# Optimization experiments

Hardware: AMD Instinct MI355X
Metric: run time of the kernel (lower is better)

The kernel has to match this reference:

```python
import jax, jax.numpy as jnp
import numpy as np

T = 512        # sequence / max_length
I = 512        # input_dim
H = 1024       # hidden_size
O = 1          # output_size
L = 512        # max_length (attention logits)


def setup_inputs() -> dict:
    key = jax.random.key(0)
    ks = jax.random.split(key, 14)
    s = 0.02
    return {
        "input_seq": jax.random.normal(ks[0], (T, I), jnp.float32),
        "target_seq": jax.random.normal(ks[1], (T, O), jnp.float32),
        # encoder LSTM (input I -> hidden H), PyTorch gate order i,f,g,o
        "W_ih_e": jax.random.normal(ks[2], (4 * H, I), jnp.float32) * s,
        "W_hh_e": jax.random.normal(ks[3], (4 * H, H), jnp.float32) * s,
        "b_ih_e": jnp.zeros((4 * H,), jnp.float32),
        "b_hh_e": jnp.zeros((4 * H,), jnp.float32),
        # attention: Linear(2H -> L)
        "W_attn": jax.random.normal(ks[4], (L, 2 * H), jnp.float32) * s,
        "b_attn": jnp.zeros((L,), jnp.float32),
        # decoder LSTM (input 2H -> hidden H)
        "W_ih_d": jax.random.normal(ks[5], (4 * H, 2 * H), jnp.float32) * s,
        "W_hh_d": jax.random.normal(ks[6], (4 * H, H), jnp.float32) * s,
        "b_ih_d": jnp.zeros((4 * H,), jnp.float32),
        "b_hh_d": jnp.zeros((4 * H,), jnp.float32),
        # output Linear(H -> O)
        "W_out": jax.random.normal(ks[7], (O, H), jnp.float32) * s,
        "b_out": jnp.zeros((O,), jnp.float32),
    }


def _lstm_cell(x, h, c, Wih, Whh, bih, bhh):
    gates = Wih @ x + bih + Whh @ h + bhh          # [4H]
    i, f, g, o = jnp.split(gates, 4)
    c = jax.nn.sigmoid(f) * c + jax.nn.sigmoid(i) * jnp.tanh(g)
    h = jax.nn.sigmoid(o) * jnp.tanh(c)
    return h, c


def reference(input_seq, target_seq, W_ih_e, W_hh_e, b_ih_e, b_hh_e,
              W_attn, b_attn, W_ih_d, W_hh_d, b_ih_d, b_hh_d, W_out, b_out):
    Th = input_seq.shape[0]
    max_len = W_attn.shape[0]
    hid = W_hh_e.shape[1]

    def step(carry, xs):
        eh, ec, dh, dc, aw = carry
        x_t, i = xs
        eh, ec = _lstm_cell(x_t, eh, ec, W_ih_e, W_hh_e, b_ih_e, b_hh_e)
        energy = W_attn @ jnp.concatenate([eh, dh]) + b_attn   # [L]
        aw = aw.at[i].set(energy[i])
        aw = jax.nn.softmax(aw)                                 # re-softmaxed each step, as in source
        context = aw[i] * eh                                    # [H]
        din = jnp.concatenate([context, dh])                    # [2H]
        dh, dc = _lstm_cell(din, dh, dc, W_ih_d, W_hh_d, b_ih_d, b_hh_d)
        out_t = W_out @ dh + b_out                              # [O]
        return (eh, ec, dh, dc, aw), out_t

    z = jnp.zeros((hid,), input_seq.dtype)
    carry0 = (z, z, z, z, jnp.zeros((max_len,), input_seq.dtype))
    _, output_seq = jax.lax.scan(step, carry0, (input_seq, jnp.arange(Th)))
    return output_seq  # [T, O]
```

## Files before the change

### kernel.cpp

```cpp
#include <hip/hip_runtime.h>
#include <math.h>


#define T_STEPS 512
#define ENC_BLK 128
#define NBLK    256
#define SPIN_LIMIT 200000u
#define REP_STRIDE ((size_t)T_STEPS * 1024)

typedef float fv4 __attribute__((ext_vector_type(4)));

__device__ __forceinline__ float sigf(float x) { return 1.0f / (1.0f + expf(-x)); }

__device__ __forceinline__ unsigned ld_u(unsigned* p) {
  return __hip_atomic_load(p, __ATOMIC_RELAXED, __HIP_MEMORY_SCOPE_AGENT);
}
__device__ __forceinline__ void st_u(unsigned* p, unsigned v) {
  __hip_atomic_store(p, v, __ATOMIC_RELAXED, __HIP_MEMORY_SCOPE_AGENT);
}

__device__ __forceinline__ fv4 ld_bypass16(const float* p) {
  fv4 v;
  asm volatile("global_load_dwordx4 %0, %1, off sc0 sc1\n\t"
               "s_waitcnt vmcnt(0)"
               : "=&v"(v) : "v"(p) : "memory");
  return v;
}
__device__ __forceinline__ void st_bypass4(float* p, float v) {
  asm volatile("global_store_dword %0, %1, off sc0 sc1"
               :: "v"(p), "v"(v) : "memory");
}

__device__ __forceinline__ bool valid4(fv4 v) {
  return __float_as_uint(v.x) != 0xAAAAAAAAu && __float_as_uint(v.y) != 0xAAAAAAAAu &&
         __float_as_uint(v.z) != 0xAAAAAAAAu && __float_as_uint(v.w) != 0xAAAAAAAAu;
}

__device__ __forceinline__ fv4 poll_data(const float* p, unsigned* abortf, int* okp) {
  fv4 v;
  unsigned spins = 0;
  int ok = 1;
  for (;;) {
    v = ld_bypass16(p);
    if (valid4(v)) break;
    ++spins;
    if (spins > 4u) __builtin_amdgcn_s_sleep(1);
    if ((spins & 63u) == 0u) {
      if (ld_u(abortf) != 0u || spins > SPIN_LIMIT) { ok = 0; break; }
    }
  }
  *okp = ok;
  return v;
}

__global__ __launch_bounds__(256) void prep_gemm(const float* __restrict__ X,
                                                 const float* __restrict__ Wih,
                                                 const float* __restrict__ bih,
                                                 const float* __restrict__ bhh,
                                                 float* __restrict__ px,
                                                 unsigned* abortf) {
  if (blockIdx.x == 0 && blockIdx.y == 0 && threadIdx.x == 0) st_u(abortf, 0u);
  __shared__ float Ws[64][68];
  __shared__ float Xs[64][68];
  const int r0 = blockIdx.x * 64;
  const int t0 = blockIdx.y * 64;
  const int tid = threadIdx.x;
  const int tr = tid & 15;
  const int tc = tid >> 4;
  float acc[4][4] = {{0.f}};
  for (int k0 = 0; k0 < 512; k0 += 64) {
    __syncthreads();
    const int lr = tid >> 4;
    const int lc = (tid & 15) * 4;
#pragma unroll
    for (int rep = 0; rep < 4; rep++) {
      const int row = lr + rep * 16;
      const float4 wv = *(const float4*)&Wih[(size_t)(r0 + row) * 512 + k0 + lc];
      Ws[lc + 0][row] = wv.x; Ws[lc + 1][row] = wv.y;
      Ws[lc + 2][row] = wv.z; Ws[lc + 3][row] = wv.w;
      const float4 xv = *(const float4*)&X[(size_t)(t0 + row) * 512 + k0 + lc];
      Xs[row][lc + 0] = xv.x; Xs[row][lc + 1] = xv.y;
      Xs[row][lc + 2] = xv.z; Xs[row][lc + 3] = xv.w;
    }
    __syncthreads();
    for (int kk = 0; kk < 64; kk++) {
      float a[4], x[4];
#pragma unroll
      for (int i = 0; i < 4; i++) a[i] = Ws[kk][tr * 4 + i];
#pragma unroll
      for (int j = 0; j < 4; j++) x[j] = Xs[tc * 4 + j][kk];
#pragma unroll
      for (int i = 0; i < 4; i++)
#pragma unroll
        for (int j = 0; j < 4; j++) acc[i][j] += a[i] * x[j];
    }
  }
#pragma unroll
  for (int i = 0; i < 4; i++) {
    const int r = r0 + tr * 4 + i;
    const int g = r >> 10, h = r & 1023;
    const float bsum = bih[r] + bhh[r];
#pragma unroll
    for (int j = 0; j < 4; j++) {
      const int t = t0 + tc * 4 + j;
      px[((size_t)t * 1024 + h) * 4 + g] = acc[i][j] + bsum;
    }
  }
}

__global__ __launch_bounds__(256, 1) void lstm_persist(
    const float* __restrict__ Whhe, const float* __restrict__ Wattn,
    const float* __restrict__ battn, const float* __restrict__ Wihd,
    const float* __restrict__ Whhd, const float* __restrict__ bihd,
    const float* __restrict__ bhhd, const float* __restrict__ Wout,
    const float* __restrict__ bout, const float* __restrict__ px,
    float* ehbuf, float* dhbuf, int nrep, unsigned* abortf, float* out) {
  __shared__ float4 xbuf[256];
  __shared__ float4 dbuf[256];
  __shared__ float  aw[512];
  __shared__ float  GA[32];
  __shared__ float  GB[32];
  __shared__ float  redE[4];
  __shared__ float  redE2[4];
  __shared__ float  red[8];
  __shared__ float  red2[4];
  __shared__ float  bd[32];
  __shared__ int    sbad;

  const int b    = blockIdx.x;
  const int tid  = threadIdx.x;
  const int w    = tid >> 6;
  const int lane = tid & 63;
  const int jj   = lane & 7;
  const int seg  = lane >> 3;
  const size_t myrep = (size_t)(b & (nrep - 1)) * REP_STRIDE;

  if (b < ENC_BLK) {
    const int e = b;
    const int r = (w << 10) + (e << 3) + jj;
    float4 we[32];
#pragma unroll
    for (int k = 0; k < 32; k++) {
      const int m = (k + seg) & 31;
      we[k] = *(const float4*)&Whhe[(size_t)r * 1024 + seg * 128 + m * 4];
    }
    xbuf[tid] = make_float4(0.f, 0.f, 0.f, 0.f);
    if (tid == 0) sbad = 0;
    float ec = 0.f;
    __syncthreads();

    for (int t = 0; t < T_STEPS; t++) {
      float pxv = 0.f;
      if (seg == 0) pxv = px[((size_t)t * 1024 + (e << 3) + jj) * 4 + w];
      float ge = 0.f;
#pragma unroll
      for (int k = 0; k < 32; k++) {
        const int m = (k + seg) & 31;
        const float4 x = xbuf[seg * 32 + m];
        ge += we[k].x * x.x + we[k].y * x.y + we[k].z * x.z + we[k].w * x.w;
      }
      ge += __shfl_xor(ge, 8, 64);
      ge += __shfl_xor(ge, 16, 64);
      ge += __shfl_xor(ge, 32, 64);
      if (seg == 0) GA[(w << 3) + jj] = ge + pxv;
      __syncthreads();
      if (tid < 8) {
        const float gi = GA[tid], gf = GA[8 + tid], gg = GA[16 + tid], go = GA[24 + tid];
        const float c = sigf(gf) * ec + sigf(gi) * tanhf(gg);
        ec = c;
        const float h = sigf(go) * tanhf(c);
        for (int rp = 0; rp < nrep; rp++)
          st_bypass4(&ehbuf[(size_t)rp * REP_STRIDE + (size_t)t * 1024 + (e << 3) + tid], h);
      }
      int ok;
      const fv4 ev = poll_data(&ehbuf[myrep + (size_t)t * 1024 + tid * 4], abortf, &ok);
      if (!ok) { st_u(abortf, 1u); sbad = 1; }
      xbuf[tid] = make_float4(ev.x, ev.y, ev.z, ev.w);
      __syncthreads();
      if (sbad) break;
    }
  } else {
    const int d = b - ENC_BLK;
    const int r = (w << 10) + (d << 3) + jj;
    float4 w1[32], wr[32];
#pragma unroll
    for (int k = 0; k < 32; k++) {
      const int m = (k + seg) & 31;
      w1[k] = *(const float4*)&Wihd[(size_t)r * 2048 + seg * 128 + m * 4];
      const float4 a = *(const float4*)&Wihd[(size_t)r * 2048 + 1024 + seg * 128 + m * 4];
      const float4 c = *(const float4*)&Whhd[(size_t)r * 1024 + seg * 128 + m * 4];
      wr[k] = make_float4(a.x + c.x, a.y + c.y, a.z + c.z, a.w + c.w);
    }
    if (tid < 32) {
      const int g = tid >> 3, j = tid & 7;
      bd[tid] = bihd[(g << 10) + (d << 3) + j] + bhhd[(g << 10) + (d << 3) + j];
    }
    xbuf[tid] = make_float4(0.f, 0.f, 0.f, 0.f);
    dbuf[tid] = make_float4(0.f, 0.f, 0.f, 0.f);
    aw[tid] = 0.f; aw[tid + 256] = 0.f;
    if (tid == 0) sbad = 0;
    float dc = 0.f;
    const float4 wo = *(const float4*)&Wout[tid * 4];
    const float boutv = bout[0];
    __syncthreads();

    bool failed = false;
    for (int t = 0; t < T_STEPS; t++) {
      const float4 wae = *(const float4*)&Wattn[(size_t)t * 2048 + tid * 4];
      const float4 wad = *(const float4*)&Wattn[(size_t)t * 2048 + 1024 + tid * 4];
      const float battn_t = battn[t];
      const float ex0 = expf(aw[tid]);
      const float ex1 = expf(aw[tid + 256]);
      float so = ((tid == t) ? 0.f : ex0) + ((tid + 256 == t) ? 0.f : ex1);
#pragma unroll
      for (int mk = 1; mk <= 32; mk <<= 1) so += __shfl_xor(so, mk, 64);
      if (lane == 0) red[w] = so;

      int ok1;
      const fv4 ev = poll_data(&ehbuf[myrep + (size_t)t * 1024 + tid * 4], abortf, &ok1);
      if (!ok1) { st_u(abortf, 1u); sbad = 1; }
      float epe = wae.x * ev.x + wae.y * ev.y + wae.z * ev.z + wae.w * ev.w;
#pragma unroll
      for (int mk = 1; mk <= 32; mk <<= 1) epe += __shfl_xor(epe, mk, 64);
      if (lane == 0) redE[w] = epe;
      xbuf[tid] = make_float4(ev.x, ev.y, ev.z, ev.w);
      __syncthreads();
      if (sbad) { failed = true; break; }

      float g1 = 0.f;
#pragma unroll
      for (int k = 0; k < 32; k++) {
        const int m = (k + seg) & 31;
        const float4 x = xbuf[seg * 32 + m];
        g1 += w1[k].x * x.x + w1[k].y * x.y + w1[k].z * x.z + w1[k].w * x.w;
      }
      g1 += __shfl_xor(g1, 8, 64); g1 += __shfl_xor(g1, 16, 64); g1 += __shfl_xor(g1, 32, 64);
      if (seg == 0) GA[(w << 3) + jj] = g1;

      fv4 dv = {0.f, 0.f, 0.f, 0.f};
      float epd = 0.f;
      if (t > 0) {
        int ok2;
        dv = poll_data(&dhbuf[myrep + (size_t)(t - 1) * 1024 + tid * 4], abortf, &ok2);
        if (!ok2) { st_u(abortf, 1u); sbad = 1; }
        epd = wad.x * dv.x + wad.y * dv.y + wad.z * dv.z + wad.w * dv.w;
      }
#pragma unroll
      for (int mk = 1; mk <= 32; mk <<= 1) epd += __shfl_xor(epd, mk, 64);
      if (lane == 0) redE2[w] = epd;
      dbuf[tid] = make_float4(dv.x, dv.y, dv.z, dv.w);
      __syncthreads();
      if (sbad) { failed = true; break; }

      float g2 = 0.f;
#pragma unroll
      for (int k = 0; k < 32; k++) {
        const int m = (k + seg) & 31;
        const float4 dd = dbuf[seg * 32 + m];
        g2 += wr[k].x * dd.x + wr[k].y * dd.y + wr[k].z * dd.z + wr[k].w * dd.w;
      }
      g2 += __shfl_xor(g2, 8, 64); g2 += __shfl_xor(g2, 16, 64); g2 += __shfl_xor(g2, 32, 64);
      if (seg == 0) GB[(w << 3) + jj] = g2;

      const float sum_other = red[0] + red[1] + red[2] + red[3];
      const float e_t = redE[0] + redE[1] + redE[2] + redE[3] +
                        redE2[0] + redE2[1] + redE2[2] + redE2[3] + battn_t;
      const float exden = expf(e_t);
      const float inv = 1.f / (sum_other + exden);
      aw[tid] = ((tid == t) ? exden : ex0) * inv;
      aw[tid + 256] = ((tid + 256 == t) ? exden : ex1) * inv;
      const float awt = exden * inv;
      __syncthreads();

      if (tid < 8) {
        const float gi = awt * GA[tid]      + GB[tid]      + bd[tid];
        const float gf = awt * GA[8 + tid]  + GB[8 + tid]  + bd[8 + tid];
        const float gg = awt * GA[16 + tid] + GB[16 + tid] + bd[16 + tid];
        const float go = awt * GA[24 + tid] + GB[24 + tid] + bd[24 + tid];
        const float c = sigf(gf) * dc + sigf(gi) * tanhf(gg);
        dc = c;
        const float h = sigf(go) * tanhf(c);
        for (int rp = 0; rp < nrep; rp++)
          st_bypass4(&dhbuf[(size_t)rp * REP_STRIDE + (size_t)t * 1024 + (d << 3) + tid], h);
      }
    }

    if (!failed) {
#pragma unroll
      for (int i = 0; i < 4; i++) {
        const int t = d * 4 + i;
        int ok;
        const fv4 dv = poll_data(&dhbuf[myrep + (size_t)t * 1024 + tid * 4], abortf, &ok);
        if (!ok) break;
        float op = wo.x * dv.x + wo.y * dv.y + wo.z * dv.z + wo.w * dv.w;
#pragma unroll
        for (int mk = 1; mk <= 32; mk <<= 1) op += __shfl_xor(op, mk, 64);
        if (lane == 0) red2[w] = op;
        __syncthreads();
        if (tid == 0) out[t] = red2[0] + red2[1] + red2[2] + red2[3] + boutv;
        __syncthreads();
      }
    }
  }
}

extern "C" void kernel_launch(void* const* d_in, const int* in_sizes, int n_in,
                              void* d_out, int out_size, void* d_ws, size_t ws_size,
                              hipStream_t stream) {
  const float* X     = (const float*)d_in[0];
  const float* Wihe  = (const float*)d_in[2];
  const float* Whhe  = (const float*)d_in[3];
  const float* bihe  = (const float*)d_in[4];
  const float* bhhe  = (const float*)d_in[5];
  const float* Wattn = (const float*)d_in[6];
  const float* battn = (const float*)d_in[7];
  const float* Wihd  = (const float*)d_in[8];
  const float* Whhd  = (const float*)d_in[9];
  const float* bihd  = (const float*)d_in[10];
  const float* bhhd  = (const float*)d_in[11];
  const float* Wo    = (const float*)d_in[12];
  const float* bo    = (const float*)d_in[13];
  float* out = (float*)d_out;

  const size_t px_elems = (size_t)T_STEPS * 1024 * 4;
  int nrep = 8;
  size_t need;
  for (;; nrep >>= 1) {
    need = (px_elems + 2 * (size_t)nrep * REP_STRIDE) * sizeof(float) + sizeof(unsigned);
    if (need <= ws_size || nrep == 1) break;
  }
  if (ws_size < need) return;

  float* ws    = (float*)d_ws;
  float* px    = ws;
  float* ehbuf = px + px_elems;
  float* dhbuf = ehbuf + (size_t)nrep * REP_STRIDE;
  unsigned* abortf = (unsigned*)(dhbuf + (size_t)nrep * REP_STRIDE);

  prep_gemm<<<dim3(64, 8), 256, 0, stream>>>(X, Wihe, bihe, bhhe, px, abortf);
  lstm_persist<<<NBLK, 256, 0, stream>>>(
      Whhe, Wattn, battn, Wihd, Whhd, bihd, bhhd, Wo, bo, px, ehbuf, dhbuf,
      nrep, abortf, out);
}
```

Measured before the change: 2.114 ms.

## Replace LDS gate exchange with shuffles, pipeline polling, drop replicas and abort flag

Row mapping changes so all four gates of a hidden unit sit in one wavefront. Gate combination therefore uses cross-lane shuffles instead of shared-memory arrays plus a block barrier, which removes a __syncthreads per step in both encoder and decoder. Polling moves to an inline-asm loop that keeps two sets of bypass loads in flight, and drops the sleep and the global abort-flag checks. The replicated eh/dh buffers are collapsed to a single copy, which cuts store traffic but concentrates all reads on one location. Double-buffered shared arrays keep the one remaining barrier per step safe.

```diff
diff --git a/kernel.cpp b/kernel.cpp
--- a/kernel.cpp
+++ b/kernel.cpp
@@ -5,61 +5,90 @@
 #define T_STEPS 512
 #define ENC_BLK 128
 #define NBLK    256
-#define SPIN_LIMIT 200000u
-#define REP_STRIDE ((size_t)T_STEPS * 1024)
 
 typedef float fv4 __attribute__((ext_vector_type(4)));
 
 __device__ __forceinline__ float sigf(float x) { return 1.0f / (1.0f + expf(-x)); }
 
-__device__ __forceinline__ unsigned ld_u(unsigned* p) {
-  return __hip_atomic_load(p, __ATOMIC_RELAXED, __HIP_MEMORY_SCOPE_AGENT);
-}
-__device__ __forceinline__ void st_u(unsigned* p, unsigned v) {
-  __hip_atomic_store(p, v, __ATOMIC_RELAXED, __HIP_MEMORY_SCOPE_AGENT);
-}
-
-__device__ __forceinline__ fv4 ld_bypass16(const float* p) {
-  fv4 v;
-  asm volatile("global_load_dwordx4 %0, %1, off sc0 sc1\n\t"
-               "s_waitcnt vmcnt(0)"
-               : "=&v"(v) : "v"(p) : "memory");
-  return v;
-}
 __device__ __forceinline__ void st_bypass4(float* p, float v) {
   asm volatile("global_store_dword %0, %1, off sc0 sc1"
                :: "v"(p), "v"(v) : "memory");
 }
 
-__device__ __forceinline__ bool valid4(fv4 v) {
-  return __float_as_uint(v.x) != 0xAAAAAAAAu && __float_as_uint(v.y) != 0xAAAAAAAAu &&
-         __float_as_uint(v.z) != 0xAAAAAAAAu && __float_as_uint(v.w) != 0xAAAAAAAAu;
-}
-
-__device__ __forceinline__ fv4 poll_data(const float* p, unsigned* abortf, int* okp) {
-  fv4 v;
-  unsigned spins = 0;
-  int ok = 1;
-  for (;;) {
-    v = ld_bypass16(p);
-    if (valid4(v)) break;
-    ++spins;
-    if (spins > 4u) __builtin_amdgcn_s_sleep(1);
-    if ((spins & 63u) == 0u) {
-      if (ld_u(abortf) != 0u || spins > SPIN_LIMIT) { ok = 0; break; }
-    }
-  }
-  *okp = ok;
-  return v;
+__device__ __forceinline__ fv4 poll_pipe(const float* p, int* okp) {
+  float a0, a1, a2, a3, b0, b1, b2, b3;
+  unsigned flag, cnt;
+  asm volatile(
+      "s_mov_b32 %8, 0\n\t"
+      "s_mov_b32 %9, 0\n\t"
+      "global_load_dword %0, %10, off sc0 sc1\n\t"
+      "global_load_dword %1, %10, off offset:4 sc0 sc1\n\t"
+      "global_load_dword %2, %10, off offset:8 sc0 sc1\n\t"
+      "global_load_dword %3, %10, off offset:12 sc0 sc1\n\t"
+      "PLA%=:\n\t"
+      "global_load_dword %4, %10, off sc0 sc1\n\t"
+      "global_load_dword %5, %10, off offset:4 sc0 sc1\n\t"
+      "global_load_dword %6, %10, off offset:8 sc0 sc1\n\t"
+      "global_load_dword %7, %10, off offset:12 sc0 sc1\n\t"
+      "s_waitcnt vmcnt(4)\n\t"
+      "v_cmp_eq_u32 vcc, 0xaaaaaaaa, %0\n\t"
+      "s_cbranch_vccnz PRB%=\n\t"
+      "v_cmp_eq_u32 vcc, 0xaaaaaaaa, %1\n\t"
+      "s_cbranch_vccnz PRB%=\n\t"
+      "v_cmp_eq_u32 vcc, 0xaaaaaaaa, %2\n\t"
+      "s_cbranch_vccnz PRB%=\n\t"
+      "v_cmp_eq_u32 vcc, 0xaaaaaaaa, %3\n\t"
+      "s_cbranch_vccnz PRB%=\n\t"
+      "s_waitcnt vmcnt(0)\n\t"
+      "s_branch PDONE%=\n\t"
+      "PRB%=:\n\t"
+      "s_add_u32 %9, %9, 1\n\t"
+      "s_cmp_lt_u32 %9, 0xc350\n\t"
+      "s_cbranch_scc0 PTO%=\n\t"
+      "global_load_dword %0, %10, off sc0 sc1\n\t"
+      "global_load_dword %1, %10, off offset:4 sc0 sc1\n\t"
+      "global_load_dword %2, %10, off offset:8 sc0 sc1\n\t"
+      "global_load_dword %3, %10, off offset:12 sc0 sc1\n\t"
+      "s_waitcnt vmcnt(4)\n\t"
+      "v_cmp_eq_u32 vcc, 0xaaaaaaaa, %4\n\t"
+      "s_cbranch_vccnz PRA%=\n\t"
+      "v_cmp_eq_u32 vcc, 0xaaaaaaaa, %5\n\t"
+      "s_cbranch_vccnz PRA%=\n\t"
+      "v_cmp_eq_u32 vcc, 0xaaaaaaaa, %6\n\t"
+      "s_cbranch_vccnz PRA%=\n\t"
+      "v_cmp_eq_u32 vcc, 0xaaaaaaaa, %7\n\t"
+      "s_cbranch_vccnz PRA%=\n\t"
+      "s_waitcnt vmcnt(0)\n\t"
+      "v_mov_b32 %0, %4\n\t"
+      "v_mov_b32 %1, %5\n\t"
+      "v_mov_b32 %2, %6\n\t"
+      "v_mov_b32 %3, %7\n\t"
+      "s_branch PDONE%=\n\t"
+      "PRA%=:\n\t"
+      "s_add_u32 %9, %9, 1\n\t"
+      "s_cmp_lt_u32 %9, 0xc350\n\t"
+      "s_cbranch_scc0 PTO%=\n\t"
+      "s_branch PLA%=\n\t"
+      "PTO%=:\n\t"
+      "s_mov_b32 %8, 1\n\t"
+      "s_waitcnt vmcnt(0)\n\t"
+      "PDONE%=:"
+      : "=&v"(a0), "=&v"(a1), "=&v"(a2), "=&v"(a3),
+        "=&v"(b0), "=&v"(b1), "=&v"(b2), "=&v"(b3),
+        "=&s"(flag), "=&s"(cnt)
+      : "v"(p)
+      : "vcc", "scc", "memory");
+  *okp = (flag == 0);
+  fv4 r;
+  r.x = a0; r.y = a1; r.z = a2; r.w = a3;
+  return r;
 }
 
 __global__ __launch_bounds__(256) void prep_gemm(const float* __restrict__ X,
                                                  const float* __restrict__ Wih,
                                                  const float* __restrict__ bih,
                                                  const float* __restrict__ bhh,
-                                                 float* __restrict__ px,
-                                                 unsigned* abortf) {
-  if (blockIdx.x == 0 && blockIdx.y == 0 && threadIdx.x == 0) st_u(abortf, 0u);
+                                                 float* __restrict__ px) {
   __shared__ float Ws[64][68];
   __shared__ float Xs[64][68];
   const int r0 = blockIdx.x * 64;
@@ -114,74 +143,72 @@
     const float* __restrict__ Whhd, const float* __restrict__ bihd,
     const float* __restrict__ bhhd, const float* __restrict__ Wout,
     const float* __restrict__ bout, const float* __restrict__ px,
-    float* ehbuf, float* dhbuf, int nrep, unsigned* abortf, float* out) {
-  __shared__ float4 xbuf[256];
-  __shared__ float4 dbuf[256];
+    float* ehbuf, float* dhbuf, float* out) {
+  __shared__ float4 xbufE[2][256];
+  __shared__ float4 xbufD[256];
+  __shared__ float4 dbufD[256];
   __shared__ float  aw[512];
-  __shared__ float  GA[32];
-  __shared__ float  GB[32];
-  __shared__ float  redE[4];
-  __shared__ float  redE2[4];
-  __shared__ float  red[8];
+  __shared__ float  redE[2][4];
+  __shared__ float  redE2[2][4];
+  __shared__ float  red[2][4];
   __shared__ float  red2[4];
-  __shared__ float  bd[32];
   __shared__ int    sbad;
 
-  const int b    = blockIdx.x;
-  const int tid  = threadIdx.x;
-  const int w    = tid >> 6;
-  const int lane = tid & 63;
-  const int jj   = lane & 7;
-  const int seg  = lane >> 3;
-  const size_t myrep = (size_t)(b & (nrep - 1)) * REP_STRIDE;
+  const int b     = blockIdx.x;
+  const int tid   = threadIdx.x;
+  const int w     = tid >> 6;
+  const int lane  = tid & 63;
+  const int idx   = lane & 7;
+  const int g     = idx >> 1;
+  const int jc    = lane & 1;
+  const int seg   = lane >> 3;
 
   if (b < ENC_BLK) {
     const int e = b;
-    const int r = (w << 10) + (e << 3) + jj;
+    const int r = (g << 10) + (e << 3) + 2 * w + (idx & 1);
     float4 we[32];
 #pragma unroll
     for (int k = 0; k < 32; k++) {
       const int m = (k + seg) & 31;
       we[k] = *(const float4*)&Whhe[(size_t)r * 1024 + seg * 128 + m * 4];
     }
-    xbuf[tid] = make_float4(0.f, 0.f, 0.f, 0.f);
+    xbufE[0][tid] = make_float4(0.f, 0.f, 0.f, 0.f);
     if (tid == 0) sbad = 0;
     float ec = 0.f;
     __syncthreads();
 
     for (int t = 0; t < T_STEPS; t++) {
-      float pxv = 0.f;
-      if (seg == 0) pxv = px[((size_t)t * 1024 + (e << 3) + jj) * 4 + w];
+      const int par = t & 1;
       float ge = 0.f;
 #pragma unroll
       for (int k = 0; k < 32; k++) {
         const int m = (k + seg) & 31;
-        const float4 x = xbuf[seg * 32 + m];
+        const float4 x = xbufE[par][seg * 32 + m];
         ge += we[k].x * x.x + we[k].y * x.y + we[k].z * x.z + we[k].w * x.w;
       }
+      if (lane < 8)
+        ge += px[((size_t)t * 1024 + (e << 3) + 2 * w + (idx & 1)) * 4 + g];
       ge += __shfl_xor(ge, 8, 64);
       ge += __shfl_xor(ge, 16, 64);
       ge += __shfl_xor(ge, 32, 64);
-      if (seg == 0) GA[(w << 3) + jj] = ge + pxv;
-      __syncthreads();
-      if (tid < 8) {
-        const float gi = GA[tid], gf = GA[8 + tid], gg = GA[16 + tid], go = GA[24 + tid];
+      const float gi = __shfl(ge, jc, 64), gf = __shfl(ge, 2 + jc, 64);
+      const float gg = __shfl(ge, 4 + jc, 64), go = __shfl(ge, 6 + jc, 64);
+      if (lane < 2) {
         const float c = sigf(gf) * ec + sigf(gi) * tanhf(gg);
         ec = c;
         const float h = sigf(go) * tanhf(c);
-        for (int rp = 0; rp < nrep; rp++)
-          st_bypass4(&ehbuf[(size_t)rp * REP_STRIDE + (size_t)t * 1024 + (e << 3) + tid], h);
+        st_bypass4(&ehbuf[(size_t)t * 1024 + (e << 3) + 2 * w + lane], h);
       }
       int ok;
-      const fv4 ev = poll_data(&ehbuf[myrep + (size_t)t * 1024 + tid * 4], abortf, &ok);
-      if (!ok) { st_u(abortf, 1u); sbad = 1; }
-      xbuf[tid] = make_float4(ev.x, ev.y, ev.z, ev.w);
+      const fv4 ev = poll_pipe(&ehbuf[(size_t)t * 1024 + tid * 4], &ok);
+      if (!ok) sbad = 1;
+      xbufE[par ^ 1][tid] = make_float4(ev.x, ev.y, ev.z, ev.w);
       __syncthreads();
       if (sbad) break;
     }
   } else {
     const int d = b - ENC_BLK;
-    const int r = (w << 10) + (d << 3) + jj;
+    const int r = (g << 10) + (d << 3) + 2 * w + (idx & 1);
     float4 w1[32], wr[32];
 #pragma unroll
     for (int k = 0; k < 32; k++) {
@@ -191,12 +218,7 @@
       const float4 c = *(const float4*)&Whhd[(size_t)r * 1024 + seg * 128 + m * 4];
       wr[k] = make_float4(a.x + c.x, a.y + c.y, a.z + c.z, a.w + c.w);
     }
-    if (tid < 32) {
-      const int g = tid >> 3, j = tid & 7;
-      bd[tid] = bihd[(g << 10) + (d << 3) + j] + bhhd[(g << 10) + (d << 3) + j];
-    }
-    xbuf[tid] = make_float4(0.f, 0.f, 0.f, 0.f);
-    dbuf[tid] = make_float4(0.f, 0.f, 0.f, 0.f);
+    const float bdreg = bihd[r] + bhhd[r];
     aw[tid] = 0.f; aw[tid + 256] = 0.f;
     if (tid == 0) sbad = 0;
     float dc = 0.f;
@@ -206,6 +228,7 @@
 
     bool failed = false;
     for (int t = 0; t < T_STEPS; t++) {
+      const int par = t & 1;
       const float4 wae = *(const float4*)&Wattn[(size_t)t * 2048 + tid * 4];
       const float4 wad = *(const float4*)&Wattn[(size_t)t * 2048 + 1024 + tid * 4];
       const float battn_t = battn[t];
@@ -214,16 +237,16 @@
       float so = ((tid == t) ? 0.f : ex0) + ((tid + 256 == t) ? 0.f : ex1);
 #pragma unroll
       for (int mk = 1; mk <= 32; mk <<= 1) so += __shfl_xor(so, mk, 64);
-      if (lane == 0) red[w] = so;
+      if (lane == 0) red[par][w] = so;
 
       int ok1;
-      const fv4 ev = poll_data(&ehbuf[myrep + (size_t)t * 1024 + tid * 4], abortf, &ok1);
-      if (!ok1) { st_u(abortf, 1u); sbad = 1; }
+      const fv4 ev = poll_pipe(&ehbuf[(size_t)t * 1024 + tid * 4], &ok1);
+      if (!ok1) sbad = 1;
       float epe = wae.x * ev.x + wae.y * ev.y + wae.z * ev.z + wae.w * ev.w;
 #pragma unroll
       for (int mk = 1; mk <= 32; mk <<= 1) epe += __shfl_xor(epe, mk, 64);
-      if (lane == 0) redE[w] = epe;
-      xbuf[tid] = make_float4(ev.x, ev.y, ev.z, ev.w);
+      if (lane == 0) redE[par][w] = epe;
+      xbufD[tid] = make_float4(ev.x, ev.y, ev.z, ev.w);
       __syncthreads();
       if (sbad) { failed = true; break; }
 
@@ -231,24 +254,25 @@
 #pragma unroll
       for (int k = 0; k < 32; k++) {
         const int m = (k + seg) & 31;
-        const float4 x = xbuf[seg * 32 + m];
+        const float4 x = xbufD[seg * 32 + m];
         g1 += w1[k].x * x.x + w1[k].y * x.y + w1[k].z * x.z + w1[k].w * x.w;
       }
-      g1 += __shfl_xor(g1, 8, 64); g1 += __shfl_xor(g1, 16, 64); g1 += __shfl_xor(g1, 32, 64);
-      if (seg == 0) GA[(w << 3) + jj] = g1;
+      g1 += __shfl_xor(g1, 8, 64);
+      g1 += __shfl_xor(g1, 16, 64);
+      g1 += __shfl_xor(g1, 32, 64);
 
       fv4 dv = {0.f, 0.f, 0.f, 0.f};
       float epd = 0.f;
       if (t > 0) {
         int ok2;
-        dv = poll_data(&dhbuf[myrep + (size_t)(t - 1) * 1024 + tid * 4], abortf, &ok2);
-        if (!ok2) { st_u(abortf, 1u); sbad = 1; }
+        dv = poll_pipe(&dhbuf[(size_t)(t - 1) * 1024 + tid * 4], &ok2);
+        if (!ok2) sbad = 1;
         epd = wad.x * dv.x + wad.y * dv.y + wad.z * dv.z + wad.w * dv.w;
       }
 #pragma unroll
       for (int mk = 1; mk <= 32; mk <<= 1) epd += __shfl_xor(epd, mk, 64);
-      if (lane == 0) redE2[w] = epd;
-      dbuf[tid] = make_float4(dv.x, dv.y, dv.z, dv.w);
+      if (lane == 0) redE2[par][w] = epd;
+      dbufD[tid] = make_float4(dv.x, dv.y, dv.z, dv.w);
       __syncthreads();
       if (sbad) { failed = true; break; }
 
@@ -256,33 +280,31 @@
 #pragma unroll
       for (int k = 0; k < 32; k++) {
         const int m = (k + seg) & 31;
-        const float4 dd = dbuf[seg * 32 + m];
+        const float4 dd = dbufD[seg * 32 + m];
         g2 += wr[k].x * dd.x + wr[k].y * dd.y + wr[k].z * dd.z + wr[k].w * dd.w;
       }
-      g2 += __shfl_xor(g2, 8, 64); g2 += __shfl_xor(g2, 16, 64); g2 += __shfl_xor(g2, 32, 64);
-      if (seg == 0) GB[(w << 3) + jj] = g2;
-
-      const float sum_other = red[0] + red[1] + red[2] + red[3];
-      const float e_t = redE[0] + redE[1] + redE[2] + redE[3] +
-                        redE2[0] + redE2[1] + redE2[2] + redE2[3] + battn_t;
+      g2 += __shfl_xor(g2, 8, 64);
+      g2 += __shfl_xor(g2, 16, 64);
+      g2 += __shfl_xor(g2, 32, 64);
+
+      const float e_t = redE[par][0] + redE[par][1] + redE[par][2] + redE[par][3] +
+                        redE2[par][0] + redE2[par][1] + redE2[par][2] + redE2[par][3] +
+                        battn_t;
       const float exden = expf(e_t);
-      const float inv = 1.f / (sum_other + exden);
-      aw[tid] = ((tid == t) ? exden : ex0) * inv;
-      aw[tid + 256] = ((tid + 256 == t) ? exden : ex1) * inv;
+      const float inv = 1.f / (red[par][0] + red[par][1] + red[par][2] + red[par][3] + exden);
       const float awt = exden * inv;
-      __syncthreads();
-
-      if (tid < 8) {
-        const float gi = awt * GA[tid]      + GB[tid]      + bd[tid];
-        const float gf = awt * GA[8 + tid]  + GB[8 + tid]  + bd[8 + tid];
-        const float gg = awt * GA[16 + tid] + GB[16 + tid] + bd[16 + tid];
-        const float go = awt * GA[24 + tid] + GB[24 + tid] + bd[24 + tid];
+
+      const float v = awt * g1 + g2 + bdreg;
+      const float gi = __shfl(v, jc, 64), gf = __shfl(v, 2 + jc, 64);
+      const float gg = __shfl(v, 4 + jc, 64), go = __shfl(v, 6 + jc, 64);
+      if (lane < 2) {
         const float c = sigf(gf) * dc + sigf(gi) * tanhf(gg);
         dc = c;
         const float h = sigf(go) * tanhf(c);
-        for (int rp = 0; rp < nrep; rp++)
-          st_bypass4(&dhbuf[(size_t)rp * REP_STRIDE + (size_t)t * 1024 + (d << 3) + tid], h);
-      }
+        st_bypass4(&dhbuf[(size_t)t * 1024 + (d << 3) + 2 * w + lane], h);
+      }
+      aw[tid] = ((tid == t) ? exden : ex0) * inv;
+      aw[tid + 256] = ((tid + 256 == t) ? exden : ex1) * inv;
     }
 
     if (!failed) {
@@ -290,7 +312,7 @@
       for (int i = 0; i < 4; i++) {
         const int t = d * 4 + i;
         int ok;
-        const fv4 dv = poll_data(&dhbuf[myrep + (size_t)t * 1024 + tid * 4], abortf, &ok);
+        const fv4 dv = poll_pipe(&dhbuf[(size_t)t * 1024 + tid * 4], &ok);
         if (!ok) break;
         float op = wo.x * dv.x + wo.y * dv.y + wo.z * dv.z + wo.w * dv.w;
 #pragma unroll
@@ -322,23 +344,14 @@
   const float* bo    = (const float*)d_in[13];
   float* out = (float*)d_out;
 
-  const size_t px_elems = (size_t)T_STEPS * 1024 * 4;
-  int nrep = 8;
-  size_t need;
-  for (;; nrep >>= 1) {
-    need = (px_elems + 2 * (size_t)nrep * REP_STRIDE) * sizeof(float) + sizeof(unsigned);
-    if (need <= ws_size || nrep == 1) break;
-  }
-  if (ws_size < need) return;
-
   float* ws    = (float*)d_ws;
   float* px    = ws;
-  float* ehbuf = px + px_elems;
-  float* dhbuf = ehbuf + (size_t)nrep * REP_STRIDE;
-  unsigned* abortf = (unsigned*)(dhbuf + (size_t)nrep * REP_STRIDE);
-
-  prep_gemm<<<dim3(64, 8), 256, 0, stream>>>(X, Wihe, bihe, bhhe, px, abortf);
+  float* ehbuf = px + (size_t)T_STEPS * 1024 * 4;
+  float* dhbuf = ehbuf + (size_t)T_STEPS * 1024;
+  const size_t need = ((size_t)T_STEPS * 1024 * 6) * sizeof(float);
+  if (ws_size < need) return;
+
+  prep_gemm<<<dim3(64, 8), 256, 0, stream>>>(X, Wihe, bihe, bhhe, px);
   lstm_persist<<<NBLK, 256, 0, stream>>>(
-      Whhe, Wattn, battn, Wihd, Whhd, bihd, bhhd, Wo, bo, px, ehbuf, dhbuf,
-      nrep, abortf, out);
-}
+      Whhe, Wattn, battn, Wihd, Whhd, bihd, bhhd, Wo, bo, px, ehbuf, dhbuf, out);
+}
```

Result: slower. 2.887 ms (+36.6%).

## Double persistent block width to 512 threads and drop replicated hidden-state buffers

Applied to the files above, without the earlier changes.

Raises the persistent LSTM kernel from 256 to 512 threads per block, halving each thread's register-resident weight slice (16 instead of 32 float4 per matrix) and splitting the dot product over 16 lanes instead of 8. Removes the nrep replication of the encoder/decoder hidden-state buffers and the abort-flag machinery, so each producer writes one copy and all consumers poll a single location. The new poll routine keeps two outstanding cache-bypassing loads in flight and drops the sleep, aiming to cut per-step handoff latency. In exchange it adds more polling contention on one buffer, and the timeout no longer propagates across blocks through a shared flag.

```diff
diff --git a/kernel.cpp b/kernel.cpp
--- a/kernel.cpp
+++ b/kernel.cpp
@@ -5,27 +5,13 @@
 #define T_STEPS 512
 #define ENC_BLK 128
 #define NBLK    256
-#define SPIN_LIMIT 200000u
-#define REP_STRIDE ((size_t)T_STEPS * 1024)
+#define NTHR    512
+#define POLL_LIMIT 30000u
 
 typedef float fv4 __attribute__((ext_vector_type(4)));
 
 __device__ __forceinline__ float sigf(float x) { return 1.0f / (1.0f + expf(-x)); }
 
-__device__ __forceinline__ unsigned ld_u(unsigned* p) {
-  return __hip_atomic_load(p, __ATOMIC_RELAXED, __HIP_MEMORY_SCOPE_AGENT);
-}
-__device__ __forceinline__ void st_u(unsigned* p, unsigned v) {
-  __hip_atomic_store(p, v, __ATOMIC_RELAXED, __HIP_MEMORY_SCOPE_AGENT);
-}
-
-__device__ __forceinline__ fv4 ld_bypass16(const float* p) {
-  fv4 v;
-  asm volatile("global_load_dwordx4 %0, %1, off sc0 sc1\n\t"
-               "s_waitcnt vmcnt(0)"
-               : "=&v"(v) : "v"(p) : "memory");
-  return v;
-}
 __device__ __forceinline__ void st_bypass4(float* p, float v) {
   asm volatile("global_store_dword %0, %1, off sc0 sc1"
                :: "v"(p), "v"(v) : "memory");
@@ -36,30 +22,28 @@
          __float_as_uint(v.z) != 0xAAAAAAAAu && __float_as_uint(v.w) != 0xAAAAAAAAu;
 }
 
-__device__ __forceinline__ fv4 poll_data(const float* p, unsigned* abortf, int* okp) {
-  fv4 v;
-  unsigned spins = 0;
+__device__ __forceinline__ fv4 poll2(const float* p, int* okp) {
+  fv4 a, b;
   int ok = 1;
-  for (;;) {
-    v = ld_bypass16(p);
-    if (valid4(v)) break;
-    ++spins;
-    if (spins > 4u) __builtin_amdgcn_s_sleep(1);
-    if ((spins & 63u) == 0u) {
-      if (ld_u(abortf) != 0u || spins > SPIN_LIMIT) { ok = 0; break; }
-    }
+  asm volatile("global_load_dwordx4 %0, %1, off sc0 sc1" : "=v"(a) : "v"(p) : "memory");
+  for (unsigned it = 0;; ++it) {
+    asm volatile("global_load_dwordx4 %0, %1, off sc0 sc1" : "=v"(b) : "v"(p) : "memory");
+    asm volatile("s_waitcnt vmcnt(1)" : "+v"(a) :: "memory");
+    if (valid4(a)) { asm volatile("s_waitcnt vmcnt(0)" ::: "memory"); break; }
+    asm volatile("global_load_dwordx4 %0, %1, off sc0 sc1" : "=v"(a) : "v"(p) : "memory");
+    asm volatile("s_waitcnt vmcnt(1)" : "+v"(b) :: "memory");
+    if (valid4(b)) { asm volatile("s_waitcnt vmcnt(0)" ::: "memory"); a = b; break; }
+    if (it > POLL_LIMIT) { ok = 0; asm volatile("s_waitcnt vmcnt(0)" ::: "memory"); break; }
   }
   *okp = ok;
-  return v;
+  return a;
 }
 
 __global__ __launch_bounds__(256) void prep_gemm(const float* __restrict__ X,
                                                  const float* __restrict__ Wih,
                                                  const float* __restrict__ bih,
                                                  const float* __restrict__ bhh,
-                                                 float* __restrict__ px,
-                                                 unsigned* abortf) {
-  if (blockIdx.x == 0 && blockIdx.y == 0 && threadIdx.x == 0) st_u(abortf, 0u);
+                                                 float* __restrict__ px) {
   __shared__ float Ws[64][68];
   __shared__ float Xs[64][68];
   const int r0 = blockIdx.x * 64;
@@ -108,168 +92,181 @@
   }
 }
 
-__global__ __launch_bounds__(256, 1) void lstm_persist(
+__global__ __launch_bounds__(512, 1) void lstm_persist(
     const float* __restrict__ Whhe, const float* __restrict__ Wattn,
     const float* __restrict__ battn, const float* __restrict__ Wihd,
     const float* __restrict__ Whhd, const float* __restrict__ bihd,
     const float* __restrict__ bhhd, const float* __restrict__ Wout,
     const float* __restrict__ bout, const float* __restrict__ px,
-    float* ehbuf, float* dhbuf, int nrep, unsigned* abortf, float* out) {
+    float* ehbuf, float* dhbuf, float* out) {
   __shared__ float4 xbuf[256];
   __shared__ float4 dbuf[256];
   __shared__ float  aw[512];
   __shared__ float  GA[32];
   __shared__ float  GB[32];
+  __shared__ float  bd[32];
   __shared__ float  redE[4];
   __shared__ float  redE2[4];
   __shared__ float  red[8];
   __shared__ float  red2[4];
-  __shared__ float  bd[32];
   __shared__ int    sbad;
 
   const int b    = blockIdx.x;
   const int tid  = threadIdx.x;
   const int w    = tid >> 6;
   const int lane = tid & 63;
-  const int jj   = lane & 7;
-  const int seg  = lane >> 3;
-  const size_t myrep = (size_t)(b & (nrep - 1)) * REP_STRIDE;
+  const int ri   = lane & 3;
+  const int s16  = lane >> 2;
+  const int g    = w >> 1;
+  const int j    = ((w & 1) << 2) + ri;
 
   if (b < ENC_BLK) {
     const int e = b;
-    const int r = (w << 10) + (e << 3) + jj;
-    float4 we[32];
-#pragma unroll
-    for (int k = 0; k < 32; k++) {
-      const int m = (k + seg) & 31;
-      we[k] = *(const float4*)&Whhe[(size_t)r * 1024 + seg * 128 + m * 4];
-    }
-    xbuf[tid] = make_float4(0.f, 0.f, 0.f, 0.f);
+    const int r = (g << 10) + (e << 3) + j;
+    float4 we[16];
+#pragma unroll
+    for (int k = 0; k < 16; k++) {
+      const int m = (k + s16) & 15;
+      we[k] = *(const float4*)&Whhe[(size_t)r * 1024 + s16 * 64 + m * 4];
+    }
+    if (tid < 256) xbuf[tid] = make_float4(0.f, 0.f, 0.f, 0.f);
     if (tid == 0) sbad = 0;
     float ec = 0.f;
     __syncthreads();
 
     for (int t = 0; t < T_STEPS; t++) {
-      float pxv = 0.f;
-      if (seg == 0) pxv = px[((size_t)t * 1024 + (e << 3) + jj) * 4 + w];
       float ge = 0.f;
 #pragma unroll
-      for (int k = 0; k < 32; k++) {
-        const int m = (k + seg) & 31;
-        const float4 x = xbuf[seg * 32 + m];
+      for (int k = 0; k < 16; k++) {
+        const int m = (k + s16) & 15;
+        const float4 x = xbuf[s16 * 16 + m];
         ge += we[k].x * x.x + we[k].y * x.y + we[k].z * x.z + we[k].w * x.w;
       }
+      if (s16 == 0) ge += px[((size_t)t * 1024 + (e << 3) + j) * 4 + g];
+      ge += __shfl_xor(ge, 4, 64);
       ge += __shfl_xor(ge, 8, 64);
       ge += __shfl_xor(ge, 16, 64);
       ge += __shfl_xor(ge, 32, 64);
-      if (seg == 0) GA[(w << 3) + jj] = ge + pxv;
+      if (lane < 4) GA[w * 4 + lane] = ge;
       __syncthreads();
       if (tid < 8) {
         const float gi = GA[tid], gf = GA[8 + tid], gg = GA[16 + tid], go = GA[24 + tid];
         const float c = sigf(gf) * ec + sigf(gi) * tanhf(gg);
         ec = c;
         const float h = sigf(go) * tanhf(c);
-        for (int rp = 0; rp < nrep; rp++)
-          st_bypass4(&ehbuf[(size_t)rp * REP_STRIDE + (size_t)t * 1024 + (e << 3) + tid], h);
-      }
-      int ok;
-      const fv4 ev = poll_data(&ehbuf[myrep + (size_t)t * 1024 + tid * 4], abortf, &ok);
-      if (!ok) { st_u(abortf, 1u); sbad = 1; }
-      xbuf[tid] = make_float4(ev.x, ev.y, ev.z, ev.w);
+        st_bypass4(&ehbuf[(size_t)t * 1024 + (e << 3) + tid], h);
+      }
+      int ok = 1;
+      if (tid < 256) {
+        const fv4 ev = poll2(&ehbuf[(size_t)t * 1024 + tid * 4], &ok);
+        xbuf[tid] = make_float4(ev.x, ev.y, ev.z, ev.w);
+      }
+      if (!ok) sbad = 1;
       __syncthreads();
       if (sbad) break;
     }
   } else {
     const int d = b - ENC_BLK;
-    const int r = (w << 10) + (d << 3) + jj;
-    float4 w1[32], wr[32];
-#pragma unroll
-    for (int k = 0; k < 32; k++) {
-      const int m = (k + seg) & 31;
-      w1[k] = *(const float4*)&Wihd[(size_t)r * 2048 + seg * 128 + m * 4];
-      const float4 a = *(const float4*)&Wihd[(size_t)r * 2048 + 1024 + seg * 128 + m * 4];
-      const float4 c = *(const float4*)&Whhd[(size_t)r * 1024 + seg * 128 + m * 4];
+    const int r = (g << 10) + (d << 3) + j;
+    float4 w1[16], wr[16];
+#pragma unroll
+    for (int k = 0; k < 16; k++) {
+      const int m = (k + s16) & 15;
+      w1[k] = *(const float4*)&Wihd[(size_t)r * 2048 + s16 * 64 + m * 4];
+      const float4 a = *(const float4*)&Wihd[(size_t)r * 2048 + 1024 + s16 * 64 + m * 4];
+      const float4 c = *(const float4*)&Whhd[(size_t)r * 1024 + s16 * 64 + m * 4];
       wr[k] = make_float4(a.x + c.x, a.y + c.y, a.z + c.z, a.w + c.w);
     }
     if (tid < 32) {
-      const int g = tid >> 3, j = tid & 7;
-      bd[tid] = bihd[(g << 10) + (d << 3) + j] + bhhd[(g << 10) + (d << 3) + j];
-    }
-    xbuf[tid] = make_float4(0.f, 0.f, 0.f, 0.f);
-    dbuf[tid] = make_float4(0.f, 0.f, 0.f, 0.f);
-    aw[tid] = 0.f; aw[tid + 256] = 0.f;
+      const int gg2 = tid >> 3, jj2 = tid & 7;
+      bd[tid] = bihd[(gg2 << 10) + (d << 3) + jj2] + bhhd[(gg2 << 10) + (d << 3) + jj2];
+    }
+    aw[tid] = 0.f;
+    if (tid < 256) {
+      xbuf[tid] = make_float4(0.f, 0.f, 0.f, 0.f);
+      dbuf[tid] = make_float4(0.f, 0.f, 0.f, 0.f);
+    }
     if (tid == 0) sbad = 0;
     float dc = 0.f;
-    const float4 wo = *(const float4*)&Wout[tid * 4];
+    float4 wo = make_float4(0.f, 0.f, 0.f, 0.f);
+    if (tid < 256) wo = *(const float4*)&Wout[tid * 4];
     const float boutv = bout[0];
     __syncthreads();
 
     bool failed = false;
     for (int t = 0; t < T_STEPS; t++) {
-      const float4 wae = *(const float4*)&Wattn[(size_t)t * 2048 + tid * 4];
-      const float4 wad = *(const float4*)&Wattn[(size_t)t * 2048 + 1024 + tid * 4];
       const float battn_t = battn[t];
       const float ex0 = expf(aw[tid]);
-      const float ex1 = expf(aw[tid + 256]);
-      float so = ((tid == t) ? 0.f : ex0) + ((tid + 256 == t) ? 0.f : ex1);
+      float so = (tid == t) ? 0.f : ex0;
 #pragma unroll
       for (int mk = 1; mk <= 32; mk <<= 1) so += __shfl_xor(so, mk, 64);
       if (lane == 0) red[w] = so;
 
-      int ok1;
-      const fv4 ev = poll_data(&ehbuf[myrep + (size_t)t * 1024 + tid * 4], abortf, &ok1);
-      if (!ok1) { st_u(abortf, 1u); sbad = 1; }
-      float epe = wae.x * ev.x + wae.y * ev.y + wae.z * ev.z + wae.w * ev.w;
+      float4 wae = make_float4(0.f, 0.f, 0.f, 0.f);
+      float4 wad = make_float4(0.f, 0.f, 0.f, 0.f);
+      float epe = 0.f;
+      int ok1 = 1;
+      if (tid < 256) {
+        wae = *(const float4*)&Wattn[(size_t)t * 2048 + tid * 4];
+        wad = *(const float4*)&Wattn[(size_t)t * 2048 + 1024 + tid * 4];
+        const fv4 ev = poll2(&ehbuf[(size_t)t * 1024 + tid * 4], &ok1);
+        epe = wae.x * ev.x + wae.y * ev.y + wae.z * ev.z + wae.w * ev.w;
+        xbuf[tid] = make_float4(ev.x, ev.y, ev.z, ev.w);
+      }
+      if (!ok1) sbad = 1;
 #pragma unroll
       for (int mk = 1; mk <= 32; mk <<= 1) epe += __shfl_xor(epe, mk, 64);
-      if (lane == 0) redE[w] = epe;
-      xbuf[tid] = make_float4(ev.x, ev.y, ev.z, ev.w);
+      if (lane == 0 && w < 4) redE[w] = epe;
       __syncthreads();
       if (sbad) { failed = true; break; }
 
       float g1 = 0.f;
 #pragma unroll
-      for (int k = 0; k < 32; k++) {
-        const int m = (k + seg) & 31;
-        const float4 x = xbuf[seg * 32 + m];
+      for (int k = 0; k < 16; k++) {
+        const int m = (k + s16) & 15;
+        const float4 x = xbuf[s16 * 16 + m];
         g1 += w1[k].x * x.x + w1[k].y * x.y + w1[k].z * x.z + w1[k].w * x.w;
       }
-      g1 += __shfl_xor(g1, 8, 64); g1 += __shfl_xor(g1, 16, 64); g1 += __shfl_xor(g1, 32, 64);
-      if (seg == 0) GA[(w << 3) + jj] = g1;
-
-      fv4 dv = {0.f, 0.f, 0.f, 0.f};
+      g1 += __shfl_xor(g1, 4, 64);
+      g1 += __shfl_xor(g1, 8, 64);
+      g1 += __shfl_xor(g1, 16, 64);
+      g1 += __shfl_xor(g1, 32, 64);
+      if (lane < 4) GA[w * 4 + lane] = g1;
+
       float epd = 0.f;
-      if (t > 0) {
-        int ok2;
-        dv = poll_data(&dhbuf[myrep + (size_t)(t - 1) * 1024 + tid * 4], abortf, &ok2);
-        if (!ok2) { st_u(abortf, 1u); sbad = 1; }
+      int ok2 = 1;
+      if (t > 0 && tid < 256) {
+        const fv4 dv = poll2(&dhbuf[(size_t)(t - 1) * 1024 + tid * 4], &ok2);
         epd = wad.x * dv.x + wad.y * dv.y + wad.z * dv.z + wad.w * dv.w;
-      }
+        dbuf[tid] = make_float4(dv.x, dv.y, dv.z, dv.w);
+      }
+      if (!ok2) sbad = 1;
 #pragma unroll
       for (int mk = 1; mk <= 32; mk <<= 1) epd += __shfl_xor(epd, mk, 64);
-      if (lane == 0) redE2[w] = epd;
-      dbuf[tid] = make_float4(dv.x, dv.y, dv.z, dv.w);
+      if (lane == 0 && w < 4) redE2[w] = epd;
       __syncthreads();
       if (sbad) { failed = true; break; }
 
       float g2 = 0.f;
 #pragma unroll
-      for (int k = 0; k < 32; k++) {
-        const int m = (k + seg) & 31;
-        const float4 dd = dbuf[seg * 32 + m];
+      for (int k = 0; k < 16; k++) {
+        const int m = (k + s16) & 15;
+        const float4 dd = dbuf[s16 * 16 + m];
         g2 += wr[k].x * dd.x + wr[k].y * dd.y + wr[k].z * dd.z + wr[k].w * dd.w;
       }
-      g2 += __shfl_xor(g2, 8, 64); g2 += __shfl_xor(g2, 16, 64); g2 += __shfl_xor(g2, 32, 64);
-      if (seg == 0) GB[(w << 3) + jj] = g2;
-
-      const float sum_other = red[0] + red[1] + red[2] + red[3];
+      g2 += __shfl_xor(g2, 4, 64);
+      g2 += __shfl_xor(g2, 8, 64);
+      g2 += __shfl_xor(g2, 16, 64);
+      g2 += __shfl_xor(g2, 32, 64);
+      if (lane < 4) GB[w * 4 + lane] = g2;
+
       const float e_t = redE[0] + redE[1] + redE[2] + redE[3] +
                         redE2[0] + redE2[1] + redE2[2] + redE2[3] + battn_t;
       const float exden = expf(e_t);
-      const float inv = 1.f / (sum_other + exden);
+      const float inv = 1.f / (red[0] + red[1] + red[2] + red[3] +
+                               red[4] + red[5] + red[6] + red[7] + exden);
+      const float awt = exden * inv;
       aw[tid] = ((tid == t) ? exden : ex0) * inv;
-      aw[tid + 256] = ((tid + 256 == t) ? exden : ex1) * inv;
-      const float awt = exden * inv;
       __syncthreads();
 
       if (tid < 8) {
@@ -280,8 +277,7 @@
         const float c = sigf(gf) * dc + sigf(gi) * tanhf(gg);
         dc = c;
         const float h = sigf(go) * tanhf(c);
-        for (int rp = 0; rp < nrep; rp++)
-          st_bypass4(&dhbuf[(size_t)rp * REP_STRIDE + (size_t)t * 1024 + (d << 3) + tid], h);
+        st_bypass4(&dhbuf[(size_t)t * 1024 + (d << 3) + tid], h);
       }
     }
 
@@ -289,13 +285,16 @@
 #pragma unroll
       for (int i = 0; i < 4; i++) {
         const int t = d * 4 + i;
-        int ok;
-        const fv4 dv = poll_data(&dhbuf[myrep + (size_t)t * 1024 + tid * 4], abortf, &ok);
+        float op = 0.f;
+        int ok = 1;
+        if (tid < 256) {
+          const fv4 dv = poll2(&dhbuf[(size_t)t * 1024 + tid * 4], &ok);
+          op = wo.x * dv.x + wo.y * dv.y + wo.z * dv.z + wo.w * dv.w;
+        }
         if (!ok) break;
-        float op = wo.x * dv.x + wo.y * dv.y + wo.z * dv.z + wo.w * dv.w;
 #pragma unroll
         for (int mk = 1; mk <= 32; mk <<= 1) op += __shfl_xor(op, mk, 64);
-        if (lane == 0) red2[w] = op;
+        if (lane == 0 && w < 4) red2[w] = op;
         __syncthreads();
         if (tid == 0) out[t] = red2[0] + red2[1] + red2[2] + red2[3] + boutv;
         __syncthreads();
@@ -322,23 +321,14 @@
   const float* bo    = (const float*)d_in[13];
   float* out = (float*)d_out;
 
-  const size_t px_elems = (size_t)T_STEPS * 1024 * 4;
-  int nrep = 8;
-  size_t need;
-  for (;; nrep >>= 1) {
-    need = (px_elems + 2 * (size_t)nrep * REP_STRIDE) * sizeof(float) + sizeof(unsigned);
-    if (need <= ws_size || nrep == 1) break;
-  }
-  if (ws_size < need) return;
-
   float* ws    = (float*)d_ws;
   float* px    = ws;
-  float* ehbuf = px + px_elems;
-  float* dhbuf = ehbuf + (size_t)nrep * REP_STRIDE;
-  unsigned* abortf = (unsigned*)(dhbuf + (size_t)nrep * REP_STRIDE);
-
-  prep_gemm<<<dim3(64, 8), 256, 0, stream>>>(X, Wihe, bihe, bhhe, px, abortf);
-  lstm_persist<<<NBLK, 256, 0, stream>>>(
-      Whhe, Wattn, battn, Wihd, Whhd, bihd, bhhd, Wo, bo, px, ehbuf, dhbuf,
-      nrep, abortf, out);
-}
+  float* ehbuf = px + (size_t)T_STEPS * 1024 * 4;
+  float* dhbuf = ehbuf + (size_t)T_STEPS * 1024;
+  const size_t need = ((size_t)T_STEPS * 1024 * 6) * sizeof(float);
+  if (ws_size < need) return;
+
+  prep_gemm<<<dim3(64, 8), 256, 0, stream>>>(X, Wihe, bihe, bhhe, px);
+  lstm_persist<<<NBLK, NTHR, 0, stream>>>(
+      Whhe, Wattn, battn, Wihd, Whhd, bihd, bhhd, Wo, bo, px, ehbuf, dhbuf, out);
+}
```

Result: faster. 1.999 ms (-5.4%).
